# Kernel optimization log

Hardware: AMD Instinct MI355X
Metric: run time of the kernel (lower is better)

The kernel has to match this reference:

```python
import jax, jax.numpy as jnp
import numpy as np

KQ_DIM = 132  # latent_dim == kq_dim so gather covers full rows
EPS = 1e-12


def setup_inputs() -> dict:
    key = jax.random.key(0)
    ks = jax.random.split(key, 8)
    B, C, H, W = 8, 3, 128, 128
    N, K, D = 2048, 32, KQ_DIM
    indices = jax.random.randint(ks[0], (3, B, N, K), 0, H * W + 1, dtype=jnp.int32)
    img = jax.random.normal(ks[1], (B, C, H, W), dtype=jnp.float32)
    # stand-in backbone: 3x3 conv (ResidualDenseNetwork not in source)
    conv_w = jax.random.normal(ks[2], (D, C, 3, 3), dtype=jnp.float32) * (1.0 / np.sqrt(C * 9))
    conv_b = jnp.zeros((D,), dtype=jnp.float32)
    sc = 1.0 / np.sqrt(D)
    ks_w = jax.random.normal(ks[3], (D, D), dtype=jnp.float32) * sc
    ks_b = jax.random.normal(ks[4], (D,), dtype=jnp.float32) * sc
    qs_w = jax.random.normal(ks[5], (D, D), dtype=jnp.float32) * sc
    qs_b = jax.random.normal(ks[6], (D,), dtype=jnp.float32) * sc
    return {"indices": indices, "img": img, "conv_w": conv_w, "conv_b": conv_b,
            "ks_w": ks_w, "ks_b": ks_b, "qs_w": qs_w, "qs_b": qs_b}


def reference(indices, img, conv_w, conv_b, ks_w, ks_b, qs_w, qs_b):
    _, B, N, K = indices.shape
    # backbone conv: [B, D, H, W]
    feat = jax.lax.conv_general_dilated(
        img, conv_w, window_strides=(1, 1), padding='SAME',
        dimension_numbers=('NCHW', 'OIHW', 'NCHW')) + conv_b[None, :, None, None]
    # torch F.normalize(dim=-1) BEFORE permute -> L2 over last spatial (width) axis
    norm = jnp.linalg.norm(feat, axis=-1, keepdims=True)
    feat = feat / jnp.maximum(norm, EPS)
    # permute(0,2,3,1): [B, H, W, D] -> flatten spatial
    feat = jnp.transpose(feat, (0, 2, 3, 1))
    Bf, Hh, Ww, D = feat.shape
    flat = feat.reshape(Bf, Hh * Ww, D)
    flat = jnp.concatenate([flat, jnp.zeros((Bf, 1, D), dtype=flat.dtype)], axis=1)
    flat_ks = flat @ ks_w.T + ks_b  # [B, WH+1, D]
    flat_qs = flat @ qs_w.T + qs_b
    x_idx = indices[1].reshape(B, N * K)  # [B, N*K]
    y_idx = indices[2].reshape(B, N * K)
    x_feat = jnp.take_along_axis(flat_ks, x_idx[:, :, None], axis=1).reshape(B, N, K, D)
    y_feat = jnp.take_along_axis(flat_qs, y_idx[:, :, None], axis=1).reshape(B, N, K, D)
    # entailment logits: scaled dot product over feature dim
    logits = (x_feat * y_feat).sum(axis=-1) * (D ** -0.5)  # [B, N, K]
    return logits
```

## Files before the change

### kernel.cpp

```cpp
#include <hip/hip_runtime.h>
#include <hip/hip_bf16.h>
#include <math.h>

#define B_ 8
#define H_ 128
#define W_ 128
#define C_ 3
#define D_ 132
#define HW_ (H_*W_)
#define RPB_ (HW_+1)
#define NROWS_ (B_*RPB_)
#define AROWS_ 131136
#define FSTRIDE_ 136
#define MSTRIDE_ 168
#define MROWS_ 136
#define MELEMS_ (MROWS_*MSTRIDE_)
#define MALLOC_ 23040
#define NK_ 65536
#define NOUT_ (B_*NK_)

typedef __attribute__((ext_vector_type(8))) short short8v;
typedef __attribute__((ext_vector_type(8))) unsigned short ushort8v;
typedef __attribute__((ext_vector_type(4))) float f32x4;

#define GLOAD16(gp, lp) __builtin_amdgcn_global_load_lds( \
  (const __attribute__((address_space(1))) unsigned int*)(gp), \
  (__attribute__((address_space(3))) unsigned int*)(void*)(lp), 16, 0, 0)

__device__ inline float bf2f(unsigned short u) {
  return __uint_as_float(((unsigned)u) << 16);
}
__device__ inline unsigned short f2bf(float f) {
  __hip_bfloat16 hb = __float2bfloat16(f);
  return *(unsigned short*)&hb;
}

__global__ __launch_bounds__(512) void prep_kernel(
    const float* __restrict__ ks_w, const float* __restrict__ ks_b,
    const float* __restrict__ qs_w, const float* __restrict__ qs_b,
    unsigned short* __restrict__ Mb, float* __restrict__ cc) {
  int idx = blockIdx.x * 512 + threadIdx.x;
  if (idx >= MALLOC_) return;
  float val = 0.f;
  if (idx < MELEMS_) {
    int a = idx / MSTRIDE_;
    int k = idx - a * MSTRIDE_;
    if (k < D_) {
      if (a < D_) {
        for (int o = 0; o < D_; ++o)
          val = fmaf(ks_w[o * D_ + a], qs_w[o * D_ + k], val);
      } else if (a == 132) {
        for (int o = 0; o < D_; ++o)
          val = fmaf(qs_b[o], ks_w[o * D_ + k], val);
      } else if (a == 133) {
        for (int o = 0; o < D_; ++o)
          val = fmaf(ks_b[o], qs_w[o * D_ + k], val);
      }
    }
  }
  Mb[idx] = f2bf(val);
  if (idx == 0) {
    float s = 0.f;
    for (int o = 0; o < D_; ++o) s = fmaf(ks_b[o], qs_b[o], s);
    cc[0] = s;
  }
}

__device__ __forceinline__ float conv_item16(
    const float* __restrict__ in_s, const float* __restrict__ w_s,
    float bias, int d, int w0, float* acc) {
  float wt[27];
#pragma unroll
  for (int j = 0; j < 27; ++j) wt[j] = w_s[d * 27 + j];
#pragma unroll
  for (int i = 0; i < 16; ++i) acc[i] = bias;
#pragma unroll
  for (int ck = 0; ck < 9; ++ck) {
    const float4* p4 = (const float4*)(in_s + ck * 132);
    float v[20];
#pragma unroll
    for (int j = 0; j < 5; ++j) {
      float4 t4 = p4[(w0 >> 2) + j];
      v[4 * j + 0] = t4.x; v[4 * j + 1] = t4.y;
      v[4 * j + 2] = t4.z; v[4 * j + 3] = t4.w;
    }
#pragma unroll
    for (int i = 0; i < 16; ++i) {
      float a0 = fmaf(v[i], wt[ck * 3 + 0], acc[i]);
      float a1 = fmaf(v[i + 1], wt[ck * 3 + 1], a0);
      acc[i] = fmaf(v[i + 2], wt[ck * 3 + 2], a1);
    }
  }
  float ssq = 0.f;
#pragma unroll
  for (int i = 0; i < 16; ++i) ssq = fmaf(acc[i], acc[i], ssq);
  return ssq;
}

__global__ __launch_bounds__(512, 4) void fused_conv_gemm_kernel(
    const float* __restrict__ img, const float* __restrict__ cw,
    const float* __restrict__ cb, unsigned short* __restrict__ fmain,
    unsigned short* __restrict__ ft, const unsigned short* __restrict__ Mb,
    const float* __restrict__ cc, unsigned short* __restrict__ zmain,
    unsigned short* __restrict__ zt) {
  int bid = blockIdx.x;
  int tid = threadIdx.x;

  if (bid == B_ * H_) {
    float cval = cc[0];
    for (int i = tid; i < B_ * 128; i += 512) {
      int b = i >> 7, c = i & 127;
      size_t r = (size_t)b * RPB_ + HW_;
      fmain[r * 128 + c] = 0;
      zmain[r * 128 + c] = 0;
    }
    if (tid < B_) {
      size_t r = (size_t)tid * RPB_ + HW_;
      ushort8v f8 = {0, 0, 0, 0, 0x3F80, 0, 0, 0};
      *(ushort8v*)(ft + r * 8) = f8;
      ushort8v z8 = {0, 0, 0, 0, f2bf(cval), 0x3F80, 0, 0};
      *(ushort8v*)(zt + r * 8) = z8;
    }
    return;
  }

  int wave = tid >> 6, lane = tid & 63;
  __shared__ __align__(16) unsigned short Ms[MALLOC_];
  __shared__ __align__(16) float nscale[132];
  __shared__ __align__(16) char un[34880];
  float* in_s = (float*)un;
  float* w_s  = in_s + 9 * 132;
  float* b_s  = w_s + 132 * 27;
  float* parts = b_s + 132;
  unsigned short* As = (unsigned short*)un;
  unsigned short* su_s = (unsigned short*)nscale;

  for (int ch = wave; ch < 45; ch += 8)
    GLOAD16(Mb + (size_t)ch * 512 + lane * 8, Ms + ch * 512);

  int b = bid >> 7, h = bid & 127;
  for (int i = tid; i < 9 * 132; i += 512) {
    int ck = i / 132, x = i - ck * 132;
    int c = ck / 3, kh = ck - c * 3;
    int hh = h + kh - 1, ww = x - 1;
    float val = 0.f;
    if (x >= 1 && x <= 128 && hh >= 0 && hh < H_)
      val = img[((size_t)(b * C_ + c) * H_ + hh) * W_ + ww];
    in_s[i] = val;
  }
  for (int i = tid; i < D_ * 27; i += 512) w_s[i] = cw[i];
  if (tid < D_) b_s[tid] = cb[tid];
  __syncthreads();

  float acc0[16], acc1[16], acc2[16];
  int i0 = tid, i1 = tid + 512;
  int wg0 = i0 / 132, dd0 = i0 - wg0 * 132;
  int wg1 = i1 / 132, dd1 = i1 - wg1 * 132;
  parts[wg0 * 132 + dd0] = conv_item16(in_s, w_s, b_s[dd0], dd0, wg0 * 16, acc0);
  parts[wg1 * 132 + dd1] = conv_item16(in_s, w_s, b_s[dd1], dd1, wg1 * 16, acc1);
  int dd2 = 0;
  if (tid < 32) {
    dd2 = 100 + tid;
    parts[7 * 132 + dd2] = conv_item16(in_s, w_s, b_s[dd2], dd2, 112, acc2);
  }
  __syncthreads();
  if (tid < 132) {
    float s = 0.f;
#pragma unroll
    for (int rr = 0; rr < 8; ++rr) s += parts[rr * 132 + tid];
    nscale[tid] = 1.f / fmaxf(sqrtf(s), 1e-12f);
  }
  __syncthreads();

  {
    float sc = nscale[dd0];
#pragma unroll
    for (int i = 0; i < 16; ++i)
      As[(wg0 * 16 + i) * FSTRIDE_ + dd0] = f2bf(acc0[i] * sc);
    sc = nscale[dd1];
#pragma unroll
    for (int i = 0; i < 16; ++i)
      As[(wg1 * 16 + i) * FSTRIDE_ + dd1] = f2bf(acc1[i] * sc);
  }
  if (tid < 32) {
    float sc = nscale[dd2];
#pragma unroll
    for (int i = 0; i < 16; ++i)
      As[(112 + i) * FSTRIDE_ + dd2] = f2bf(acc2[i] * sc);
  }
  if (tid < 128) {
    uint2 tv; tv.x = 0x3F80u; tv.y = 0u;
    *(uint2*)&As[tid * FSTRIDE_ + 132] = tv;
  }
  if (tid < 32) As[128 * FSTRIDE_ + tid] = 0;
  __syncthreads();

  size_t rowbase = (size_t)b * RPB_ + (size_t)h * W_;
  unsigned short* fmb = fmain + rowbase * 128;
  for (int i2 = tid; i2 < 2048; i2 += 512) {
    int r = i2 >> 4, c8 = i2 & 15;
    *(ushort8v*)(fmb + r * 128 + c8 * 8) = *(const ushort8v*)(As + r * FSTRIDE_ + c8 * 8);
  }
  uint2 ftl = {0, 0};
  if (tid < 128) ftl = *(const uint2*)&As[tid * FSTRIDE_ + 128];

  int c15 = lane & 15, kg = lane >> 4;
  const unsigned short* arow = As + (wave * 16 + c15) * FSTRIDE_ + kg * 8;
  const unsigned short* brow = Ms + c15 * MSTRIDE_ + kg * 8;
  f32x4 acc[9] = {};
#pragma unroll
  for (int ks = 0; ks < 5; ++ks) {
    short8v af = *(const short8v*)(arow + ks * 32);
#pragma unroll
    for (int ct = 0; ct < 9; ++ct) {
      short8v bf = *(const short8v*)(brow + ct * 16 * MSTRIDE_ + ks * 32);
      acc[ct] = __builtin_amdgcn_mfma_f32_16x16x32_bf16(af, bf, acc[ct], 0, 0, 0);
    }
  }
  __syncthreads();

  float cval = cc[0];
  int r0 = wave * 16 + kg * 4;
#pragma unroll
  for (int ct = 0; ct < 9; ++ct) {
    int col = ct * 16 + c15;
#pragma unroll
    for (int j = 0; j < 4; ++j) {
      int r = r0 + j;
      if (col < D_)            As[r * FSTRIDE_ + col] = f2bf(acc[ct][j]);
      else if (col == 132)     su_s[r] = f2bf(acc[ct][j]);
      else if (col == 133)     As[r * FSTRIDE_ + 132] = f2bf(acc[ct][j] + cval);
      else if (col == 134)     As[r * FSTRIDE_ + 133] = 0x3F80;
      else if (col == 135)     As[r * FSTRIDE_ + 134] = 0;
      else if (col == 136)     As[r * FSTRIDE_ + 135] = 0;
    }
  }
  __syncthreads();

  unsigned short* zmb = zmain + rowbase * 128;
  for (int i2 = tid; i2 < 2048; i2 += 512) {
    int r = i2 >> 4, c8 = i2 & 15;
    *(ushort8v*)(zmb + r * 128 + c8 * 8) = *(const ushort8v*)(As + r * FSTRIDE_ + c8 * 8);
  }
  if (tid < 128) {
    *(ushort8v*)(zt + (rowbase + tid) * 8) = *(const ushort8v*)(As + tid * FSTRIDE_ + 128);
    ushort8v f8;
    f8[0] = (unsigned short)(ftl.x & 0xFFFFu);
    f8[1] = (unsigned short)(ftl.x >> 16);
    f8[2] = (unsigned short)(ftl.y & 0xFFFFu);
    f8[3] = (unsigned short)(ftl.y >> 16);
    f8[4] = 0x3F80;
    f8[5] = su_s[tid];
    f8[6] = 0;
    f8[7] = 0;
    *(ushort8v*)(ft + (rowbase + tid) * 8) = f8;
  }
}

__global__ __launch_bounds__(256) void gather_kernel(
    const int* __restrict__ xi, const int* __restrict__ yi,
    const unsigned short* __restrict__ fmain, const unsigned short* __restrict__ ft,
    const unsigned short* __restrict__ zmain, const unsigned short* __restrict__ zt,
    float* __restrict__ out) {
  const float scale = 0.08703882797784892f;
  int bi = blockIdx.x;
  int b = bi & 7;
  int chunk = bi >> 3;
  int lane = threadIdx.x & 7;
  int rem1 = chunk * 32 + (threadIdx.x >> 3);
  int rem2 = rem1 + 32768;

  size_t ib1 = (size_t)b * NK_ + rem1;
  size_t ib2 = (size_t)b * NK_ + rem2;
  int x1 = xi[ib1], y1 = yi[ib1];
  int x2 = xi[ib2], y2 = yi[ib2];
  size_t bbase = (size_t)b * RPB_;
  const unsigned short* fx1 = fmain + (bbase + x1) * 128;
  const unsigned short* zy1 = zmain + (bbase + y1) * 128;
  const unsigned short* fx2 = fmain + (bbase + x2) * 128;
  const unsigned short* zy2 = zmain + (bbase + y2) * 128;

  int e0 = lane * 16;
  ushort8v a10 = *(const ushort8v*)(fx1 + e0);
  ushort8v a11 = *(const ushort8v*)(fx1 + e0 + 8);
  ushort8v z10 = *(const ushort8v*)(zy1 + e0);
  ushort8v z11 = *(const ushort8v*)(zy1 + e0 + 8);
  ushort8v a20 = *(const ushort8v*)(fx2 + e0);
  ushort8v a21 = *(const ushort8v*)(fx2 + e0 + 8);
  ushort8v z20 = *(const ushort8v*)(zy2 + e0);
  ushort8v z21 = *(const ushort8v*)(zy2 + e0 + 8);
  ushort8v a1t, z1t, a2t, z2t;
  if (lane == 0) {
    a1t = *(const ushort8v*)(ft + (bbase + x1) * 8);
    z1t = *(const ushort8v*)(zt + (bbase + y1) * 8);
    a2t = *(const ushort8v*)(ft + (bbase + x2) * 8);
    z2t = *(const ushort8v*)(zt + (bbase + y2) * 8);
  }

  float acc1 = 0.f, acc2 = 0.f;
#pragma unroll
  for (int t = 0; t < 8; ++t) {
    acc1 = fmaf(bf2f(a10[t]), bf2f(z10[t]), acc1);
    acc2 = fmaf(bf2f(a20[t]), bf2f(z20[t]), acc2);
  }
#pragma unroll
  for (int t = 0; t < 8; ++t) {
    acc1 = fmaf(bf2f(a11[t]), bf2f(z11[t]), acc1);
    acc2 = fmaf(bf2f(a21[t]), bf2f(z21[t]), acc2);
  }
  if (lane == 0) {
#pragma unroll
    for (int t = 0; t < 8; ++t) {
      acc1 = fmaf(bf2f(a1t[t]), bf2f(z1t[t]), acc1);
      acc2 = fmaf(bf2f(a2t[t]), bf2f(z2t[t]), acc2);
    }
  }
  acc1 += __shfl_xor(acc1, 1);
  acc2 += __shfl_xor(acc2, 1);
  acc1 += __shfl_xor(acc1, 2);
  acc2 += __shfl_xor(acc2, 2);
  acc1 += __shfl_xor(acc1, 4);
  acc2 += __shfl_xor(acc2, 4);
  if (lane == 0) {
    out[((size_t)b << 16) | rem1] = acc1 * scale;
    out[((size_t)b << 16) | rem2] = acc2 * scale;
  }
}

extern "C" void kernel_launch(void* const* d_in, const int* in_sizes, int n_in,
                              void* d_out, int out_size, void* d_ws, size_t ws_size,
                              hipStream_t stream) {
  const int* indices  = (const int*)d_in[0];
  const float* img    = (const float*)d_in[1];
  const float* conv_w = (const float*)d_in[2];
  const float* conv_b = (const float*)d_in[3];
  const float* ks_w   = (const float*)d_in[4];
  const float* ks_b   = (const float*)d_in[5];
  const float* qs_w   = (const float*)d_in[6];
  const float* qs_b   = (const float*)d_in[7];
  float* out = (float*)d_out;

  char* w = (char*)d_ws;
  unsigned short* fmain = (unsigned short*)w;
  size_t off = (size_t)AROWS_ * 128 * 2;
  unsigned short* zmain = (unsigned short*)(w + off); off += (size_t)AROWS_ * 128 * 2;
  unsigned short* ftl = (unsigned short*)(w + off);   off += (size_t)AROWS_ * 8 * 2;
  unsigned short* ztl = (unsigned short*)(w + off);   off += (size_t)AROWS_ * 8 * 2;
  unsigned short* Mb = (unsigned short*)(w + off);    off += MALLOC_ * 2;
  float* cc = (float*)(w + off);

  const int* xi = indices + (size_t)B_ * NK_;
  const int* yi = indices + (size_t)2 * B_ * NK_;

  hipLaunchKernelGGL(prep_kernel, dim3(MALLOC_ / 512), dim3(512), 0, stream,
                     ks_w, ks_b, qs_w, qs_b, Mb, cc);
  hipLaunchKernelGGL(fused_conv_gemm_kernel, dim3(B_ * H_ + 1), dim3(512), 0, stream,
                     img, conv_w, conv_b, fmain, ftl, Mb, cc, zmain, ztl);
  hipLaunchKernelGGL(gather_kernel, dim3(NOUT_ / 64), dim3(256), 0, stream,
                     xi, yi, fmain, ftl, zmain, ztl, out);
}
```

Measured before the change: 80.78 us.

## Split fused conv+GEMM kernel into separate conv and GEMM kernels

Splits the fused conv-normalize-GEMM kernel into two kernels. The conv kernel drops the large M tile from LDS and raises its launch bound to 6 waves-per-EU occupancy. A new GEMM kernel reloads the bf16 features from global memory through direct-to-LDS loads into an XOR-swizzled tile, avoiding bank conflicts. In exchange it adds a kernel launch and a global round trip of the feature tensor. The ft column 5 is now written directly to global memory by the GEMM kernel, after the conv kernel has already stored the rest of the row.

```diff
diff --git a/kernel.cpp b/kernel.cpp
--- a/kernel.cpp
+++ b/kernel.cpp
@@ -11,7 +11,7 @@
 #define RPB_ (HW_+1)
 #define NROWS_ (B_*RPB_)
 #define AROWS_ 131136
-#define FSTRIDE_ 136
+#define ASTRIDE_ 136
 #define MSTRIDE_ 168
 #define MROWS_ 136
 #define MELEMS_ (MROWS_*MSTRIDE_)
@@ -97,12 +97,11 @@
   return ssq;
 }
 
-__global__ __launch_bounds__(512, 4) void fused_conv_gemm_kernel(
+__global__ __launch_bounds__(512, 6) void conv_kernel(
     const float* __restrict__ img, const float* __restrict__ cw,
     const float* __restrict__ cb, unsigned short* __restrict__ fmain,
-    unsigned short* __restrict__ ft, const unsigned short* __restrict__ Mb,
-    const float* __restrict__ cc, unsigned short* __restrict__ zmain,
-    unsigned short* __restrict__ zt) {
+    unsigned short* __restrict__ ft, const float* __restrict__ cc,
+    unsigned short* __restrict__ zmain, unsigned short* __restrict__ zt) {
   int bid = blockIdx.x;
   int tid = threadIdx.x;
 
@@ -124,19 +123,13 @@
     return;
   }
 
-  int wave = tid >> 6, lane = tid & 63;
-  __shared__ __align__(16) unsigned short Ms[MALLOC_];
   __shared__ __align__(16) float nscale[132];
-  __shared__ __align__(16) char un[34880];
+  __shared__ __align__(16) char un[34816];
   float* in_s = (float*)un;
   float* w_s  = in_s + 9 * 132;
   float* b_s  = w_s + 132 * 27;
   float* parts = b_s + 132;
   unsigned short* As = (unsigned short*)un;
-  unsigned short* su_s = (unsigned short*)nscale;
-
-  for (int ch = wave; ch < 45; ch += 8)
-    GLOAD16(Mb + (size_t)ch * 512 + lane * 8, Ms + ch * 512);
 
   int b = bid >> 7, h = bid & 127;
   for (int i = tid; i < 9 * 132; i += 512) {
@@ -176,84 +169,115 @@
     float sc = nscale[dd0];
 #pragma unroll
     for (int i = 0; i < 16; ++i)
-      As[(wg0 * 16 + i) * FSTRIDE_ + dd0] = f2bf(acc0[i] * sc);
+      As[(wg0 * 16 + i) * ASTRIDE_ + dd0] = f2bf(acc0[i] * sc);
     sc = nscale[dd1];
 #pragma unroll
     for (int i = 0; i < 16; ++i)
-      As[(wg1 * 16 + i) * FSTRIDE_ + dd1] = f2bf(acc1[i] * sc);
+      As[(wg1 * 16 + i) * ASTRIDE_ + dd1] = f2bf(acc1[i] * sc);
   }
   if (tid < 32) {
     float sc = nscale[dd2];
 #pragma unroll
     for (int i = 0; i < 16; ++i)
-      As[(112 + i) * FSTRIDE_ + dd2] = f2bf(acc2[i] * sc);
+      As[(112 + i) * ASTRIDE_ + dd2] = f2bf(acc2[i] * sc);
   }
   if (tid < 128) {
     uint2 tv; tv.x = 0x3F80u; tv.y = 0u;
-    *(uint2*)&As[tid * FSTRIDE_ + 132] = tv;
-  }
-  if (tid < 32) As[128 * FSTRIDE_ + tid] = 0;
+    *(uint2*)&As[tid * ASTRIDE_ + 132] = tv;
+  }
   __syncthreads();
 
   size_t rowbase = (size_t)b * RPB_ + (size_t)h * W_;
   unsigned short* fmb = fmain + rowbase * 128;
-  for (int i2 = tid; i2 < 2048; i2 += 512) {
-    int r = i2 >> 4, c8 = i2 & 15;
-    *(ushort8v*)(fmb + r * 128 + c8 * 8) = *(const ushort8v*)(As + r * FSTRIDE_ + c8 * 8);
-  }
-  uint2 ftl = {0, 0};
-  if (tid < 128) ftl = *(const uint2*)&As[tid * FSTRIDE_ + 128];
+  for (int i2 = tid; i2 < 2176; i2 += 512) {
+    if (i2 < 2048) {
+      int r = i2 >> 4, m = i2 & 15;
+      *(ushort8v*)(fmb + r * 128 + m * 8) = *(const ushort8v*)(As + r * ASTRIDE_ + m * 8);
+    } else {
+      int r = i2 - 2048;
+      *(ushort8v*)(ft + (rowbase + r) * 8) = *(const ushort8v*)(As + r * ASTRIDE_ + 128);
+    }
+  }
+}
+
+__global__ __launch_bounds__(512, 4) void gemm_kernel(
+    const unsigned short* __restrict__ fmain, unsigned short* __restrict__ ft,
+    const unsigned short* __restrict__ Mb, const float* __restrict__ cc,
+    unsigned short* __restrict__ zmain, unsigned short* __restrict__ zt) {
+  int bid = blockIdx.x;
+  int tid = threadIdx.x, wave = tid >> 6, lane = tid & 63;
+  __shared__ __align__(16) unsigned short Ms[MALLOC_];
+  __shared__ __align__(16) unsigned short As[128 * 128];
+  __shared__ __align__(16) unsigned short ftile[128 * 8];
+
+  int b = bid >> 7, h = bid & 127;
+  size_t rowbase = (size_t)b * RPB_ + (size_t)h * W_;
+
+  for (int ch = wave; ch < 45; ch += 8)
+    GLOAD16(Mb + (size_t)ch * 512 + lane * 8, Ms + ch * 512);
+  {
+    int rloc = lane >> 4, m = lane & 15;
+    for (int ch = wave; ch < 32; ch += 8) {
+      int r = ch * 4 + rloc;
+      int msrc = m ^ (r & 7);
+      GLOAD16(fmain + (rowbase + r) * 128 + msrc * 8, As + ch * 512);
+    }
+  }
+  for (int ch2 = wave; ch2 < 2; ch2 += 8)
+    GLOAD16(ft + (rowbase + ch2 * 64 + lane) * 8, ftile + ch2 * 512);
+  __syncthreads();
 
   int c15 = lane & 15, kg = lane >> 4;
-  const unsigned short* arow = As + (wave * 16 + c15) * FSTRIDE_ + kg * 8;
+  int ra = wave * 16 + c15;
   const unsigned short* brow = Ms + c15 * MSTRIDE_ + kg * 8;
   f32x4 acc[9] = {};
 #pragma unroll
-  for (int ks = 0; ks < 5; ++ks) {
-    short8v af = *(const short8v*)(arow + ks * 32);
+  for (int ks = 0; ks < 4; ++ks) {
+    int cj = ks * 4 + kg;
+    short8v af = *(const short8v*)(As + ra * 128 + ((cj ^ (ra & 7)) * 8));
 #pragma unroll
     for (int ct = 0; ct < 9; ++ct) {
       short8v bf = *(const short8v*)(brow + ct * 16 * MSTRIDE_ + ks * 32);
       acc[ct] = __builtin_amdgcn_mfma_f32_16x16x32_bf16(af, bf, acc[ct], 0, 0, 0);
     }
   }
-  __syncthreads();
+  {
+    short8v af = *(const short8v*)(ftile + ra * 8);
+#pragma unroll
+    for (int ct = 0; ct < 9; ++ct) {
+      short8v bf = *(const short8v*)(brow + ct * 16 * MSTRIDE_ + 4 * 32);
+      acc[ct] = __builtin_amdgcn_mfma_f32_16x16x32_bf16(af, bf, acc[ct], 0, 0, 0);
+    }
+  }
 
   float cval = cc[0];
-  int r0 = wave * 16 + kg * 4;
+  int r0l = wave * 16 + kg * 4;
 #pragma unroll
   for (int ct = 0; ct < 9; ++ct) {
     int col = ct * 16 + c15;
 #pragma unroll
     for (int j = 0; j < 4; ++j) {
-      int r = r0 + j;
-      if (col < D_)            As[r * FSTRIDE_ + col] = f2bf(acc[ct][j]);
-      else if (col == 132)     su_s[r] = f2bf(acc[ct][j]);
-      else if (col == 133)     As[r * FSTRIDE_ + 132] = f2bf(acc[ct][j] + cval);
-      else if (col == 134)     As[r * FSTRIDE_ + 133] = 0x3F80;
-      else if (col == 135)     As[r * FSTRIDE_ + 134] = 0;
-      else if (col == 136)     As[r * FSTRIDE_ + 135] = 0;
-    }
-  }
-  __syncthreads();
+      int r = r0l + j;
+      if (col < 128)
+        As[r * 128 + (((col >> 3) ^ (r & 7)) << 3) + (col & 7)] = f2bf(acc[ct][j]);
+      else if (col < 132)      ftile[r * 8 + (col - 128)] = f2bf(acc[ct][j]);
+      else if (col == 132)     ft[(rowbase + r) * 8 + 5] = f2bf(acc[ct][j]);
+      else if (col == 133)     ftile[r * 8 + 4] = f2bf(acc[ct][j] + cval);
+      else if (col == 134)     ftile[r * 8 + 5] = 0x3F80;
+      else if (col == 135)     ftile[r * 8 + 6] = 0;
+      else if (col == 136)     ftile[r * 8 + 7] = 0;
+    }
+  }
 
   unsigned short* zmb = zmain + rowbase * 128;
-  for (int i2 = tid; i2 < 2048; i2 += 512) {
-    int r = i2 >> 4, c8 = i2 & 15;
-    *(ushort8v*)(zmb + r * 128 + c8 * 8) = *(const ushort8v*)(As + r * FSTRIDE_ + c8 * 8);
-  }
-  if (tid < 128) {
-    *(ushort8v*)(zt + (rowbase + tid) * 8) = *(const ushort8v*)(As + tid * FSTRIDE_ + 128);
-    ushort8v f8;
-    f8[0] = (unsigned short)(ftl.x & 0xFFFFu);
-    f8[1] = (unsigned short)(ftl.x >> 16);
-    f8[2] = (unsigned short)(ftl.y & 0xFFFFu);
-    f8[3] = (unsigned short)(ftl.y >> 16);
-    f8[4] = 0x3F80;
-    f8[5] = su_s[tid];
-    f8[6] = 0;
-    f8[7] = 0;
-    *(ushort8v*)(ft + (rowbase + tid) * 8) = f8;
+  for (int i2 = lane; i2 < 256; i2 += 64) {
+    int r = wave * 16 + (i2 >> 4), m = i2 & 15;
+    *(ushort8v*)(zmb + r * 128 + m * 8) =
+        *(const ushort8v*)(As + r * 128 + ((m ^ (r & 7)) * 8));
+  }
+  if (lane < 16) {
+    int r = wave * 16 + lane;
+    *(ushort8v*)(zt + (rowbase + r) * 8) = *(const ushort8v*)(ftile + r * 8);
   }
 }
 
@@ -354,8 +378,10 @@
 
   hipLaunchKernelGGL(prep_kernel, dim3(MALLOC_ / 512), dim3(512), 0, stream,
                      ks_w, ks_b, qs_w, qs_b, Mb, cc);
-  hipLaunchKernelGGL(fused_conv_gemm_kernel, dim3(B_ * H_ + 1), dim3(512), 0, stream,
-                     img, conv_w, conv_b, fmain, ftl, Mb, cc, zmain, ztl);
+  hipLaunchKernelGGL(conv_kernel, dim3(B_ * H_ + 1), dim3(512), 0, stream,
+                     img, conv_w, conv_b, fmain, ftl, cc, zmain, ztl);
+  hipLaunchKernelGGL(gemm_kernel, dim3(B_ * H_), dim3(512), 0, stream,
+                     fmain, ftl, Mb, cc, zmain, ztl);
   hipLaunchKernelGGL(gather_kernel, dim3(NOUT_ / 64), dim3(256), 0, stream,
                      xi, yi, fmain, ftl, zmain, ztl, out);
 }
```

After: 85.91 us. 1.06x slower.
